# Kernel optimization log

Hardware: AMD Instinct MI355X
Metric: run time of the kernel (lower is better)

The kernel has to match this reference:

```python
import jax, jax.numpy as jnp
import numpy as np

N = 50000
E = 800000
IN_F = 128
OUT_F = 128


def setup_inputs() -> dict:
    key = jax.random.key(0)
    k1, k2, k3, k4, k5 = jax.random.split(key, 5)
    x = jax.random.normal(k1, (N, IN_F), dtype=jnp.float32)
    # sparse adjacency as COO edge list: row = dst (aggregating node), col = src
    edge_index = jax.random.randint(k2, (2, E), 0, N, dtype=jnp.int64)
    edge_weight = jax.random.uniform(k3, (E,), dtype=jnp.float32)
    # nn.Linear(in_features, out_features): W is [out, in], b is [out]
    W = jax.random.normal(k4, (OUT_F, IN_F), dtype=jnp.float32) * (1.0 / np.sqrt(IN_F))
    b = jax.random.normal(k5, (OUT_F,), dtype=jnp.float32) * 0.01
    return {"x": x, "edge_index": edge_index, "edge_weight": edge_weight, "W": W, "b": b}


def reference(x, edge_index, edge_weight, W, b):
    # hidden = self.linear(x)  -> [N, out]
    hidden = jnp.einsum("ni,oi->no", x, W) + b
    # out = adj @ hidden (SpMM): out[dst] += w_e * hidden[src]
    dst = edge_index[0]
    src = edge_index[1]
    msgs = edge_weight[:, None] * hidden[src]  # [E, out]
    out = jax.ops.segment_sum(msgs, dst, num_segments=x.shape[0])
    return out
```

## Files before the change

### kernel.cpp

```cpp
#include <hip/hip_runtime.h>
#include <hip/hip_bf16.h>

#define N_NODES 50000
#define N_EDGES 800000
#define FEAT    128
#define N_TILES (N_NODES / 16)
#define GEMM_BLOCKS 784
#define MAXD    32
#define OVF_CAP 16384
#define NODES_PER_GRP 6250
#define CHUNK   2048
#define NCHUNK  ((N_EDGES + CHUNK - 1) / CHUNK)
#define QCAP    110000
#define SCAT_BPG 98

using short8  = __attribute__((ext_vector_type(8))) short;
using float4v = __attribute__((ext_vector_type(4))) float;


__device__ __forceinline__ unsigned short f2b(float f) {
    __hip_bfloat16 h = __float2bfloat16(f);
    return __builtin_bit_cast(unsigned short, h);
}

__global__ __launch_bounds__(256) void k_prep(const float* __restrict__ W,
                                              int* __restrict__ ws_ints,
                                              unsigned short* __restrict__ wbf) {
    const int gid = blockIdx.x * 256 + threadIdx.x;
    if (gid < 12576) ((int4*)ws_ints)[gid] = make_int4(0, 0, 0, 0);
    if (gid < 2048) {
        const int r  = gid >> 4;
        const int cc = gid & 15;
        const float* s = W + (size_t)r * FEAT + cc * 8;
        float4v a0 = *(const float4v*)(s);
        float4v a1 = *(const float4v*)(s + 4);
        short8 v;
        #pragma unroll
        for (int j = 0; j < 4; ++j) { v[j] = (short)f2b(a0[j]); v[4 + j] = (short)f2b(a1[j]); }
        const int dst = r * 16 + (cc ^ (r & 7));
        *(short8*)(wbf + (size_t)dst * 8) = v;
    }
}

__global__ __launch_bounds__(256) void k_fused(const float* __restrict__ x,
                                               const unsigned short* __restrict__ wbf,
                                               const float* __restrict__ bias,
                                               unsigned short* __restrict__ hidden,
                                               const int* __restrict__ ei,
                                               const float* __restrict__ wt,
                                               int* __restrict__ flag,
                                               int2* __restrict__ queue) {
    __shared__ __align__(16) unsigned short Wlds[128 * 128];
    const int t = threadIdx.x;

    if (blockIdx.x < GEMM_BLOCKS) {
        #pragma unroll
        for (int j = 0; j < 8; ++j) {
            const int c16 = j * 256 + t;
            *(short8*)&Wlds[c16 * 8] = *(const short8*)(wbf + (size_t)c16 * 8);
        }
        __syncthreads();

        const int wave = t >> 6;
        const int lane = t & 63;
        int tile = blockIdx.x * 4 + wave;
        if (tile >= N_TILES) tile = N_TILES - 1;
        const int rowBase = tile * 16;
        const int m    = lane & 15;
        const int quad = lane >> 4;

        float4v acc[8];
        #pragma unroll
        for (int i = 0; i < 8; ++i) acc[i] = (float4v){0.f, 0.f, 0.f, 0.f};

        #pragma unroll
        for (int kk = 0; kk < 4; ++kk) {
            const int k0 = kk * 32 + quad * 8;
            const float* ap = x + (size_t)(rowBase + m) * FEAT + k0;
            float4v a0 = *(const float4v*)(ap);
            float4v a1 = *(const float4v*)(ap + 4);
            short8 af;
            #pragma unroll
            for (int j = 0; j < 4; ++j) { af[j] = (short)f2b(a0[j]); af[4 + j] = (short)f2b(a1[j]); }
            const int cc = kk * 4 + quad;
            #pragma unroll
            for (int nt = 0; nt < 8; ++nt) {
                const int rr = nt * 16 + m;
                short8 bf = *(const short8*)&Wlds[rr * 128 + ((cc ^ (rr & 7)) << 3)];
                acc[nt] = __builtin_amdgcn_mfma_f32_16x16x32_bf16(af, bf, acc[nt], 0, 0, 0);
            }
        }

        const int r0 = rowBase + quad * 4;
        #pragma unroll
        for (int nt = 0; nt < 8; ++nt) {
            const int col = nt * 16 + m;
            const float bc = bias[col];
            #pragma unroll
            for (int r = 0; r < 4; ++r) {
                hidden[(size_t)(r0 + r) * FEAT + col] = f2b(acc[nt][r] + bc);
            }
        }
    } else {
        int* lcnt  = (int*)Wlds;
        int* gbase = lcnt + 8;
        const int bid  = blockIdx.x - GEMM_BLOCKS;
        const int lane = t & 63;

        unsigned long long mball = __ballot(ei[2 * lane + 1] != 0);
        const int sh = (mball == 0ULL) ? 1 : 0;

        if (t < 8) lcnt[t] = 0;
        __syncthreads();

        const int e0 = bid * CHUNK + t;
        int      dstv[8];
        unsigned recv_[8];
        int      lpos[8];
        #pragma unroll
        for (int i = 0; i < 8; ++i) {
            int e = e0 + i * 256;
            if (e < N_EDGES) {
                int dst = ei[(size_t)e << sh];
                if ((unsigned)dst >= N_NODES) dst = 0;
                int src = ei[(size_t)(N_EDGES + e) << sh];
                if ((unsigned)src >= N_NODES) src = 0;
                dstv[i]  = dst;
                recv_[i] = ((unsigned)f2b(wt[e]) << 16) | (unsigned)src;
                lpos[i]  = atomicAdd(&lcnt[dst / NODES_PER_GRP], 1);
            } else {
                dstv[i] = -1;
            }
        }
        __syncthreads();
        if (t < 8) gbase[t] = atomicAdd(&flag[16 + 16 * t], lcnt[t]);
        __syncthreads();

        #pragma unroll
        for (int i = 0; i < 8; ++i) {
            if (dstv[i] < 0) continue;
            int g   = dstv[i] / NODES_PER_GRP;
            int idx = gbase[g] + lpos[i];
            if (idx < QCAP) {
                int2 r; r.x = dstv[i]; r.y = (int)recv_[i];
                queue[(size_t)g * QCAP + idx] = r;
            }
        }
    }
}

__global__ __launch_bounds__(256) void k_scat(const int2* __restrict__ queue,
                                              int* __restrict__ flag,
                                              int* __restrict__ fill,
                                              unsigned int* __restrict__ slots,
                                              int2* __restrict__ ovf) {
    const int g = blockIdx.x & 7;
    const int b = blockIdx.x >> 3;
    int n = flag[16 + 16 * g]; if (n > QCAP) n = QCAP;
    const int2* q = queue + (size_t)g * QCAP;
    const int stride = SCAT_BPG * 256;

    int i = b * 256 + (int)threadIdx.x;
    for (; i + 3 * stride < n; i += 4 * stride) {
        int2 e0 = q[i];
        int2 e1 = q[i + stride];
        int2 e2 = q[i + 2 * stride];
        int2 e3 = q[i + 3 * stride];
        int p0 = atomicAdd(&fill[e0.x], 1);
        int p1 = atomicAdd(&fill[e1.x], 1);
        int p2 = atomicAdd(&fill[e2.x], 1);
        int p3 = atomicAdd(&fill[e3.x], 1);
        if (p0 < MAXD) slots[(size_t)e0.x * MAXD + p0] = (unsigned)e0.y;
        else { int op = atomicAdd(&flag[1], 1); if (op < OVF_CAP) ovf[op] = e0; }
        if (p1 < MAXD) slots[(size_t)e1.x * MAXD + p1] = (unsigned)e1.y;
        else { int op = atomicAdd(&flag[1], 1); if (op < OVF_CAP) ovf[op] = e1; }
        if (p2 < MAXD) slots[(size_t)e2.x * MAXD + p2] = (unsigned)e2.y;
        else { int op = atomicAdd(&flag[1], 1); if (op < OVF_CAP) ovf[op] = e2; }
        if (p3 < MAXD) slots[(size_t)e3.x * MAXD + p3] = (unsigned)e3.y;
        else { int op = atomicAdd(&flag[1], 1); if (op < OVF_CAP) ovf[op] = e3; }
    }
    for (; i < n; i += stride) {
        int2 ent = q[i];
        int pos = atomicAdd(&fill[ent.x], 1);
        if (pos < MAXD) slots[(size_t)ent.x * MAXD + pos] = (unsigned)ent.y;
        else { int op = atomicAdd(&flag[1], 1); if (op < OVF_CAP) ovf[op] = ent; }
    }
}

#define AGG_FMA(w_, h_)                                                      \
    acc[0] = fmaf(w_, __uint_as_float((h_.x & 0xffffu) << 16), acc[0]);      \
    acc[1] = fmaf(w_, __uint_as_float(h_.x & 0xffff0000u),     acc[1]);      \
    acc[2] = fmaf(w_, __uint_as_float((h_.y & 0xffffu) << 16), acc[2]);      \
    acc[3] = fmaf(w_, __uint_as_float(h_.y & 0xffff0000u),     acc[3]);      \
    acc[4] = fmaf(w_, __uint_as_float((h_.z & 0xffffu) << 16), acc[4]);      \
    acc[5] = fmaf(w_, __uint_as_float(h_.z & 0xffff0000u),     acc[5]);      \
    acc[6] = fmaf(w_, __uint_as_float((h_.w & 0xffffu) << 16), acc[6]);      \
    acc[7] = fmaf(w_, __uint_as_float(h_.w & 0xffff0000u),     acc[7]);

__global__ __launch_bounds__(256) void k_agg(const int* __restrict__ fill,
                                             const unsigned int* __restrict__ slots,
                                             const unsigned int* __restrict__ hid,
                                             const int* __restrict__ flag,
                                             const int2* __restrict__ ovf,
                                             float* __restrict__ out) {
    const int wave = threadIdx.x >> 6;
    const int lane = threadIdx.x & 63;
    const int node = blockIdx.x * 4 + wave;
    const int grp  = lane >> 4;
    const int sub  = lane & 15;

    const int degf = fill[node];
    const int deg  = (degf > MAXD) ? MAXD : degf;
    const uint4* sl4 = (const uint4*)(slots + (size_t)node * MAXD);

    float acc[8];
    #pragma unroll
    for (int j = 0; j < 8; ++j) acc[j] = 0.f;

    const int iters = (deg + 3) >> 2;
    for (int it = 0; it < iters; it += 4) {
        uint4 r0 = sl4[it];
        uint4 r1 = sl4[(it + 1) & 7];
        uint4 r2 = sl4[(it + 2) & 7];
        uint4 r3 = sl4[(it + 3) & 7];
        unsigned rc0 = (grp < 2) ? (grp == 0 ? r0.x : r0.y) : (grp == 2 ? r0.z : r0.w);
        unsigned rc1 = (grp < 2) ? (grp == 0 ? r1.x : r1.y) : (grp == 2 ? r1.z : r1.w);
        unsigned rc2 = (grp < 2) ? (grp == 0 ? r2.x : r2.y) : (grp == 2 ? r2.z : r2.w);
        unsigned rc3 = (grp < 2) ? (grp == 0 ? r3.x : r3.y) : (grp == 2 ? r3.z : r3.w);
        const int e0 = it * 4 + grp;
        const bool v0 = (e0)      < deg;
        const bool v1 = (e0 + 4)  < deg;
        const bool v2 = (e0 + 8)  < deg;
        const bool v3 = (e0 + 12) < deg;
        const float w0 = v0 ? __uint_as_float(rc0 & 0xffff0000u) : 0.f;
        const float w1 = v1 ? __uint_as_float(rc1 & 0xffff0000u) : 0.f;
        const float w2 = v2 ? __uint_as_float(rc2 & 0xffff0000u) : 0.f;
        const float w3 = v3 ? __uint_as_float(rc3 & 0xffff0000u) : 0.f;
        const unsigned s0 = v0 ? (rc0 & 0xffffu) : 0u;
        const unsigned s1 = v1 ? (rc1 & 0xffffu) : 0u;
        const unsigned s2 = v2 ? (rc2 & 0xffffu) : 0u;
        const unsigned s3 = v3 ? (rc3 & 0xffffu) : 0u;
        uint4 h0 = *((const uint4*)(hid + (size_t)s0 * 64) + sub);
        uint4 h1 = *((const uint4*)(hid + (size_t)s1 * 64) + sub);
        uint4 h2 = *((const uint4*)(hid + (size_t)s2 * 64) + sub);
        uint4 h3 = *((const uint4*)(hid + (size_t)s3 * 64) + sub);
        AGG_FMA(w0, h0)
        AGG_FMA(w1, h1)
        AGG_FMA(w2, h2)
        AGG_FMA(w3, h3)
    }

    if (degf > MAXD) {
        int n = flag[1]; if (n > OVF_CAP) n = OVF_CAP;
        for (int i = 0; i < n; ++i) {
            int2 r = ovf[i];
            if (r.x != node || (i & 3) != grp) continue;
            unsigned rec = (unsigned)r.y;
            float w = __uint_as_float(rec & 0xffff0000u);
            unsigned src = rec & 0xffffu;
            uint4 h = *((const uint4*)(hid + (size_t)src * 64) + sub);
            AGG_FMA(w, h)
        }
    }

    #pragma unroll
    for (int j = 0; j < 8; ++j) {
        float a = acc[j];
        a += __shfl_xor(a, 16, 64);
        a += __shfl_xor(a, 32, 64);
        acc[j] = a;
    }

    if (lane < 16) {
        float* o = out + (size_t)node * FEAT + sub * 8;
        *(float4*)(o)     = make_float4(acc[0], acc[1], acc[2], acc[3]);
        *(float4*)(o + 4) = make_float4(acc[4], acc[5], acc[6], acc[7]);
    }
}

extern "C" void kernel_launch(void* const* d_in, const int* in_sizes, int n_in,
                              void* d_out, int out_size, void* d_ws, size_t ws_size,
                              hipStream_t stream) {
    const float* x  = (const float*)d_in[0];
    const int*   ei = (const int*)d_in[1];
    const float* ew = (const float*)d_in[2];
    const float* W  = (const float*)d_in[3];
    const float* b  = (const float*)d_in[4];
    float* out = (float*)d_out;

    int*  flag = (int*)d_ws;
    int*  fill = flag + 256;
    int2* ovf  = (int2*)(fill + 50048);
    unsigned int* slots = (unsigned int*)(ovf + OVF_CAP);
    unsigned short* hidden = (unsigned short*)(slots + (size_t)N_NODES * MAXD);
    int2* queue = (int2*)(hidden + (size_t)N_NODES * FEAT);
    unsigned short* wbf = (unsigned short*)(queue + (size_t)8 * QCAP);

    k_prep <<<64, 256, 0, stream>>>(W, flag, wbf);
    k_fused<<<GEMM_BLOCKS + NCHUNK, 256, 0, stream>>>(x, wbf, b, hidden, ei, ew,
                                                      flag, queue);
    k_scat <<<8 * SCAT_BPG, 256, 0, stream>>>(queue, flag, fill, slots, ovf);
    k_agg  <<<N_NODES / 4, 256, 0, stream>>>(fill, slots, (const unsigned int*)hidden,
                                             flag, ovf, out);
}
```

Baseline: 166.9 us.

## Slice hidden features into 16-column panels and aggregate per slice

The GEMM epilogue now writes the bf16 hidden matrix as 8 column slices of 16 features each (slice-major), so each slice is 1.6 MB. The aggregation kernel gives each block one slice and grid-strides over nodes, so the gather working set per slice can stay in L2/LLC, and it uses non-temporal loads and stores for the streaming slot and output data. The cost is that every slice re-reads the slot lists, and gathers become 4-byte loads instead of 16-byte loads.

New measurement: 249.7 us. +49.6%, slower.

```diff
diff --git a/kernel.cpp b/kernel.cpp
--- a/kernel.cpp
+++ b/kernel.cpp
@@ -13,6 +13,8 @@
 #define NCHUNK  ((N_EDGES + CHUNK - 1) / CHUNK)
 #define QCAP    110000
 #define SCAT_BPG 98
+#define AGG_QB  1563
+#define SLICE_U 400000
 
 using short8  = __attribute__((ext_vector_type(8))) short;
 using float4v = __attribute__((ext_vector_type(4))) float;
@@ -96,9 +98,10 @@
         for (int nt = 0; nt < 8; ++nt) {
             const int col = nt * 16 + m;
             const float bc = bias[col];
+            unsigned short* hp = hidden + (size_t)nt * 800000 + (size_t)r0 * 16 + m;
             #pragma unroll
             for (int r = 0; r < 4; ++r) {
-                hidden[(size_t)(r0 + r) * FEAT + col] = f2b(acc[nt][r] + bc);
+                hp[r * 16] = f2b(acc[nt][r] + bc);
             }
         }
     } else {
@@ -187,94 +190,72 @@
     }
 }
 
-#define AGG_FMA(w_, h_)                                                      \
-    acc[0] = fmaf(w_, __uint_as_float((h_.x & 0xffffu) << 16), acc[0]);      \
-    acc[1] = fmaf(w_, __uint_as_float(h_.x & 0xffff0000u),     acc[1]);      \
-    acc[2] = fmaf(w_, __uint_as_float((h_.y & 0xffffu) << 16), acc[2]);      \
-    acc[3] = fmaf(w_, __uint_as_float(h_.y & 0xffff0000u),     acc[3]);      \
-    acc[4] = fmaf(w_, __uint_as_float((h_.z & 0xffffu) << 16), acc[4]);      \
-    acc[5] = fmaf(w_, __uint_as_float(h_.z & 0xffff0000u),     acc[5]);      \
-    acc[6] = fmaf(w_, __uint_as_float((h_.w & 0xffffu) << 16), acc[6]);      \
-    acc[7] = fmaf(w_, __uint_as_float(h_.w & 0xffff0000u),     acc[7]);
-
 __global__ __launch_bounds__(256) void k_agg(const int* __restrict__ fill,
                                              const unsigned int* __restrict__ slots,
                                              const unsigned int* __restrict__ hid,
                                              const int* __restrict__ flag,
                                              const int2* __restrict__ ovf,
                                              float* __restrict__ out) {
-    const int wave = threadIdx.x >> 6;
-    const int lane = threadIdx.x & 63;
-    const int node = blockIdx.x * 4 + wave;
-    const int grp  = lane >> 4;
-    const int sub  = lane & 15;
-
-    const int degf = fill[node];
-    const int deg  = (degf > MAXD) ? MAXD : degf;
-    const uint4* sl4 = (const uint4*)(slots + (size_t)node * MAXD);
-
-    float acc[8];
-    #pragma unroll
-    for (int j = 0; j < 8; ++j) acc[j] = 0.f;
-
-    const int iters = (deg + 3) >> 2;
-    for (int it = 0; it < iters; it += 4) {
-        uint4 r0 = sl4[it];
-        uint4 r1 = sl4[(it + 1) & 7];
-        uint4 r2 = sl4[(it + 2) & 7];
-        uint4 r3 = sl4[(it + 3) & 7];
-        unsigned rc0 = (grp < 2) ? (grp == 0 ? r0.x : r0.y) : (grp == 2 ? r0.z : r0.w);
-        unsigned rc1 = (grp < 2) ? (grp == 0 ? r1.x : r1.y) : (grp == 2 ? r1.z : r1.w);
-        unsigned rc2 = (grp < 2) ? (grp == 0 ? r2.x : r2.y) : (grp == 2 ? r2.z : r2.w);
-        unsigned rc3 = (grp < 2) ? (grp == 0 ? r3.x : r3.y) : (grp == 2 ? r3.z : r3.w);
-        const int e0 = it * 4 + grp;
-        const bool v0 = (e0)      < deg;
-        const bool v1 = (e0 + 4)  < deg;
-        const bool v2 = (e0 + 8)  < deg;
-        const bool v3 = (e0 + 12) < deg;
-        const float w0 = v0 ? __uint_as_float(rc0 & 0xffff0000u) : 0.f;
-        const float w1 = v1 ? __uint_as_float(rc1 & 0xffff0000u) : 0.f;
-        const float w2 = v2 ? __uint_as_float(rc2 & 0xffff0000u) : 0.f;
-        const float w3 = v3 ? __uint_as_float(rc3 & 0xffff0000u) : 0.f;
-        const unsigned s0 = v0 ? (rc0 & 0xffffu) : 0u;
-        const unsigned s1 = v1 ? (rc1 & 0xffffu) : 0u;
-        const unsigned s2 = v2 ? (rc2 & 0xffffu) : 0u;
-        const unsigned s3 = v3 ? (rc3 & 0xffffu) : 0u;
-        uint4 h0 = *((const uint4*)(hid + (size_t)s0 * 64) + sub);
-        uint4 h1 = *((const uint4*)(hid + (size_t)s1 * 64) + sub);
-        uint4 h2 = *((const uint4*)(hid + (size_t)s2 * 64) + sub);
-        uint4 h3 = *((const uint4*)(hid + (size_t)s3 * 64) + sub);
-        AGG_FMA(w0, h0)
-        AGG_FMA(w1, h1)
-        AGG_FMA(w2, h2)
-        AGG_FMA(w3, h3)
-    }
-
-    if (degf > MAXD) {
-        int n = flag[1]; if (n > OVF_CAP) n = OVF_CAP;
-        for (int i = 0; i < n; ++i) {
-            int2 r = ovf[i];
-            if (r.x != node || (i & 3) != grp) continue;
-            unsigned rec = (unsigned)r.y;
-            float w = __uint_as_float(rec & 0xffff0000u);
-            unsigned src = rec & 0xffffu;
-            uint4 h = *((const uint4*)(hid + (size_t)src * 64) + sub);
-            AGG_FMA(w, h)
-        }
-    }
-
-    #pragma unroll
-    for (int j = 0; j < 8; ++j) {
-        float a = acc[j];
-        a += __shfl_xor(a, 16, 64);
-        a += __shfl_xor(a, 32, 64);
-        acc[j] = a;
-    }
-
-    if (lane < 16) {
-        float* o = out + (size_t)node * FEAT + sub * 8;
-        *(float4*)(o)     = make_float4(acc[0], acc[1], acc[2], acc[3]);
-        *(float4*)(o + 4) = make_float4(acc[4], acc[5], acc[6], acc[7]);
+    const int wave  = threadIdx.x >> 6;
+    const int lane  = threadIdx.x & 63;
+    const int slice = blockIdx.x & 7;
+    const int qb    = blockIdx.x >> 3;
+    const int g8    = lane >> 3;
+    const int c2    = lane & 7;
+    const unsigned* hs = hid + (size_t)slice * SLICE_U;
+
+    int novf = -1;
+
+    for (int node = qb * 4 + wave; node < N_NODES; node += AGG_QB * 4) {
+        const int degf = __builtin_nontemporal_load(fill + node);
+        const int deg  = (degf > MAXD) ? MAXD : degf;
+        const unsigned* sl = slots + (size_t)node * MAXD;
+
+        float a0 = 0.f, a1 = 0.f;
+        const int iters = (deg + 7) >> 3;
+        for (int it = 0; it < iters; it += 2) {
+            const int ea = it * 8 + g8;
+            const int eb = ea + 8;
+            unsigned ra = __builtin_nontemporal_load(sl + ea);
+            unsigned rb = __builtin_nontemporal_load(sl + (eb & 31));
+            const bool va = ea < deg;
+            const bool vb = eb < deg;
+            const float    wa = va ? __uint_as_float(ra & 0xffff0000u) : 0.f;
+            const float    wb = vb ? __uint_as_float(rb & 0xffff0000u) : 0.f;
+            const unsigned sa = va ? (ra & 0xffffu) : 0u;
+            const unsigned sb = vb ? (rb & 0xffffu) : 0u;
+            unsigned ha = hs[(size_t)sa * 8 + c2];
+            unsigned hb = hs[(size_t)sb * 8 + c2];
+            a0 = fmaf(wa, __uint_as_float((ha & 0xffffu) << 16), a0);
+            a1 = fmaf(wa, __uint_as_float(ha & 0xffff0000u),     a1);
+            a0 = fmaf(wb, __uint_as_float((hb & 0xffffu) << 16), a0);
+            a1 = fmaf(wb, __uint_as_float(hb & 0xffff0000u),     a1);
+        }
+
+        if (degf > MAXD) {
+            if (novf < 0) { novf = flag[1]; if (novf > OVF_CAP) novf = OVF_CAP; }
+            for (int i = 0; i < novf; ++i) {
+                int2 r = ovf[i];
+                if (r.x != node || (i & 7) != g8) continue;
+                unsigned rec = (unsigned)r.y;
+                float w = __uint_as_float(rec & 0xffff0000u);
+                unsigned src = rec & 0xffffu;
+                unsigned h = hs[(size_t)src * 8 + c2];
+                a0 = fmaf(w, __uint_as_float((h & 0xffffu) << 16), a0);
+                a1 = fmaf(w, __uint_as_float(h & 0xffff0000u),     a1);
+            }
+        }
+
+        a0 += __shfl_xor(a0, 8, 64);  a1 += __shfl_xor(a1, 8, 64);
+        a0 += __shfl_xor(a0, 16, 64); a1 += __shfl_xor(a1, 16, 64);
+        a0 += __shfl_xor(a0, 32, 64); a1 += __shfl_xor(a1, 32, 64);
+
+        if (lane < 8) {
+            unsigned long long p = ((unsigned long long)__float_as_uint(a1) << 32)
+                                 | (unsigned long long)__float_as_uint(a0);
+            __builtin_nontemporal_store(p, (unsigned long long*)
+                (out + (size_t)node * FEAT + slice * 16 + c2 * 2));
+        }
     }
 }
 
@@ -300,6 +281,6 @@
     k_fused<<<GEMM_BLOCKS + NCHUNK, 256, 0, stream>>>(x, wbf, b, hidden, ei, ew,
                                                       flag, queue);
     k_scat <<<8 * SCAT_BPG, 256, 0, stream>>>(queue, flag, fill, slots, ovf);
-    k_agg  <<<N_NODES / 4, 256, 0, stream>>>(fill, slots, (const unsigned int*)hidden,
-                                             flag, ovf, out);
-}
+    k_agg  <<<AGG_QB * 8, 256, 0, stream>>>(fill, slots, (const unsigned int*)hidden,
+                                            flag, ovf, out);
+}
```

## Unroll aggregation to issue all slot gathers at once and remap blocks per node group

Applied to the files above, without the earlier changes.

The aggregation kernel now loads all 32 slot records at once and issues 8 independent hidden-row gathers per lane before any FMAs. Out-of-range slots are redirected to node 0 with zero weight. This replaces the degree-bounded loop, aiming for more memory-level parallelism on the latency-bound gather. Block indices are also interleaved across 8 node groups, presumably to match the scatter kernel's grouping (possibly XCD locality). The cost is that low-degree nodes always pay for 8 gathers, plus higher register use.

Measured after the change: 165.3 us. Within noise of the previous version (-1.0%).

```diff
diff --git a/kernel.cpp b/kernel.cpp
--- a/kernel.cpp
+++ b/kernel.cpp
@@ -13,6 +13,7 @@
 #define NCHUNK  ((N_EDGES + CHUNK - 1) / CHUNK)
 #define QCAP    110000
 #define SCAT_BPG 98
+#define AGG_QPG 1563
 
 using short8  = __attribute__((ext_vector_type(8))) short;
 using float4v = __attribute__((ext_vector_type(4))) float;
@@ -205,7 +206,11 @@
                                              float* __restrict__ out) {
     const int wave = threadIdx.x >> 6;
     const int lane = threadIdx.x & 63;
-    const int node = blockIdx.x * 4 + wave;
+    const int g    = blockIdx.x & 7;
+    const int q    = blockIdx.x >> 3;
+    const int loc  = q * 4 + wave;
+    if (loc >= NODES_PER_GRP) return;
+    const int node = g * NODES_PER_GRP + loc;
     const int grp  = lane >> 4;
     const int sub  = lane & 15;
 
@@ -217,38 +222,23 @@
     #pragma unroll
     for (int j = 0; j < 8; ++j) acc[j] = 0.f;
 
-    const int iters = (deg + 3) >> 2;
-    for (int it = 0; it < iters; it += 4) {
-        uint4 r0 = sl4[it];
-        uint4 r1 = sl4[(it + 1) & 7];
-        uint4 r2 = sl4[(it + 2) & 7];
-        uint4 r3 = sl4[(it + 3) & 7];
-        unsigned rc0 = (grp < 2) ? (grp == 0 ? r0.x : r0.y) : (grp == 2 ? r0.z : r0.w);
-        unsigned rc1 = (grp < 2) ? (grp == 0 ? r1.x : r1.y) : (grp == 2 ? r1.z : r1.w);
-        unsigned rc2 = (grp < 2) ? (grp == 0 ? r2.x : r2.y) : (grp == 2 ? r2.z : r2.w);
-        unsigned rc3 = (grp < 2) ? (grp == 0 ? r3.x : r3.y) : (grp == 2 ? r3.z : r3.w);
-        const int e0 = it * 4 + grp;
-        const bool v0 = (e0)      < deg;
-        const bool v1 = (e0 + 4)  < deg;
-        const bool v2 = (e0 + 8)  < deg;
-        const bool v3 = (e0 + 12) < deg;
-        const float w0 = v0 ? __uint_as_float(rc0 & 0xffff0000u) : 0.f;
-        const float w1 = v1 ? __uint_as_float(rc1 & 0xffff0000u) : 0.f;
-        const float w2 = v2 ? __uint_as_float(rc2 & 0xffff0000u) : 0.f;
-        const float w3 = v3 ? __uint_as_float(rc3 & 0xffff0000u) : 0.f;
-        const unsigned s0 = v0 ? (rc0 & 0xffffu) : 0u;
-        const unsigned s1 = v1 ? (rc1 & 0xffffu) : 0u;
-        const unsigned s2 = v2 ? (rc2 & 0xffffu) : 0u;
-        const unsigned s3 = v3 ? (rc3 & 0xffffu) : 0u;
-        uint4 h0 = *((const uint4*)(hid + (size_t)s0 * 64) + sub);
-        uint4 h1 = *((const uint4*)(hid + (size_t)s1 * 64) + sub);
-        uint4 h2 = *((const uint4*)(hid + (size_t)s2 * 64) + sub);
-        uint4 h3 = *((const uint4*)(hid + (size_t)s3 * 64) + sub);
-        AGG_FMA(w0, h0)
-        AGG_FMA(w1, h1)
-        AGG_FMA(w2, h2)
-        AGG_FMA(w3, h3)
-    }
+    uint4 L[8];
+    #pragma unroll
+    for (int k = 0; k < 8; ++k) L[k] = sl4[k];
+    unsigned src_[8]; float w_[8];
+    #pragma unroll
+    for (int k = 0; k < 8; ++k) {
+        unsigned rc = (grp < 2) ? (grp == 0 ? L[k].x : L[k].y)
+                                : (grp == 2 ? L[k].z : L[k].w);
+        const bool v = (k * 4 + grp) < deg;
+        w_[k]   = v ? __uint_as_float(rc & 0xffff0000u) : 0.f;
+        src_[k] = v ? (rc & 0xffffu) : 0u;
+    }
+    uint4 H[8];
+    #pragma unroll
+    for (int k = 0; k < 8; ++k) H[k] = *((const uint4*)(hid + (size_t)src_[k] * 64) + sub);
+    #pragma unroll
+    for (int k = 0; k < 8; ++k) { AGG_FMA(w_[k], H[k]) }
 
     if (degf > MAXD) {
         int n = flag[1]; if (n > OVF_CAP) n = OVF_CAP;
@@ -300,6 +290,6 @@
     k_fused<<<GEMM_BLOCKS + NCHUNK, 256, 0, stream>>>(x, wbf, b, hidden, ei, ew,
                                                       flag, queue);
     k_scat <<<8 * SCAT_BPG, 256, 0, stream>>>(queue, flag, fill, slots, ovf);
-    k_agg  <<<N_NODES / 4, 256, 0, stream>>>(fill, slots, (const unsigned int*)hidden,
+    k_agg  <<<8 * AGG_QPG, 256, 0, stream>>>(fill, slots, (const unsigned int*)hidden,
                                              flag, ovf, out);
 }
```
